# Kernel optimization log

Measured on AMD Instinct MI355X. Metric: run time of the kernel, lower is better.

The kernel has to match this reference:

```python
import jax, jax.numpy as jnp
import numpy as np

N = 50000      # nodes of type 'conn'
E = 250000     # edges per edge type
NT = 3         # number of edge types
H = 3          # num_heads for hidden layers
D1, D2, DO = 64, 64, 32
IN0 = 34       # 8 + 3 + 6 + 17


def setup_inputs() -> dict:
    key = jax.random.key(0)
    ks = jax.random.split(key, 40)
    it = iter(range(40))

    def nrm(shape, scale=0.1):
        return jax.random.normal(ks[next(it)], shape, dtype=jnp.float32) * scale

    inp = {}
    inp["cat_inputs"] = jax.random.randint(ks[next(it)], (N, 3), 0, 5, dtype=jnp.int32)
    inp["cont_inputs"] = jax.random.normal(ks[next(it)], (N, 17), dtype=jnp.float32)
    inp["src"] = jax.random.randint(ks[next(it)], (NT, E), 0, N)
    inp["dst"] = jax.random.randint(ks[next(it)], (NT, E), 0, N)
    # embedding tables
    inp["emb0"] = nrm((14, 8))
    inp["emb1"] = nrm((5, 3))
    inp["emb2"] = nrm((10, 6))
    # layer 1: GATConv(34 -> 64, heads=3) per etype
    inp["W1"] = nrm((NT, IN0, H * D1))
    inp["al1"] = nrm((NT, H, D1))
    inp["ar1"] = nrm((NT, H, D1))
    inp["b1"] = nrm((NT, H * D1))
    # layer 2: GATConv(192 -> 64, heads=3) per etype
    inp["W2"] = nrm((NT, H * D1, H * D2))
    inp["al2"] = nrm((NT, H, D2))
    inp["ar2"] = nrm((NT, H, D2))
    inp["b2"] = nrm((NT, H * D2))
    # output layer: GATConv(192 -> 32, heads=1) per etype
    inp["W3"] = nrm((NT, H * D2, DO))
    inp["al3"] = nrm((NT, 1, DO))
    inp["ar3"] = nrm((NT, 1, DO))
    inp["b3"] = nrm((NT, DO))
    return inp


def _gat(x, W, al, ar, b, src_t, dst_t, heads, out):
    """DGL GATConv: linear -> per-edge LeakyReLU(0.2) attention -> edge softmax
    over incoming edges -> weighted scatter-sum -> +bias -> leaky_relu(0.01)."""
    n = x.shape[0]
    feat = (x @ W).reshape(n, heads, out)          # (N,H,D)
    el = jnp.sum(feat * al, axis=-1)               # (N,H)
    er = jnp.sum(feat * ar, axis=-1)               # (N,H)
    e = jax.nn.leaky_relu(el[src_t] + er[dst_t], 0.2)  # (E,H)
    emax = jax.ops.segment_max(e, dst_t, num_segments=n)   # (N,H), -inf for empty ok
    ee = jnp.exp(e - emax[dst_t])
    den = jax.ops.segment_sum(ee, dst_t, num_segments=n)
    alpha = ee / den[dst_t]                        # (E,H)
    msg = feat[src_t] * alpha[:, :, None]          # (E,H,D)
    rst = jax.ops.segment_sum(msg, dst_t, num_segments=n) + b.reshape(1, heads, out)
    return jax.nn.leaky_relu(rst, 0.01)            # GATConv activation=F.leaky_relu


def reference(cont_inputs, emb0, emb1, emb2,
              W1, al1, ar1, b1, W2, al2, ar2, b2, W3, al3, ar3, b3,
              cat_inputs, src, dst):
    x = jnp.concatenate([emb0[cat_inputs[:, 0]],
                         emb1[cat_inputs[:, 1]],
                         emb2[cat_inputs[:, 2]],
                         cont_inputs], axis=1)     # (N,34)

    def hetero(h, W, al, ar, b, heads, out):
        # HeteroGraphConv(aggregate='mean') over NT edge types, then flatten(1)
        outs = [_gat(h, W[t], al[t], ar[t], b[t], src[t], dst[t], heads, out)
                for t in range(NT)]
        agg = jnp.mean(jnp.stack(outs, 0), axis=0)  # (N,heads,out)
        return agg.reshape(h.shape[0], heads * out)

    h = hetero(x, W1, al1, ar1, b1, H, D1)
    h = hetero(h, W2, al2, ar2, b2, H, D2)
    h = hetero(h, W3, al3, ar3, b3, 1, DO)
    return h
```

## Files before the change

### kernel.cpp

```cpp
#include <hip/hip_runtime.h>

#define NNODES 50000
#define NEDGES 250000
#define NTYPES 3
#define SCAN_B ((NNODES + 255) / 256)

typedef __attribute__((ext_vector_type(8))) short bf16x8;
typedef __attribute__((ext_vector_type(4))) float f32x4;

__device__ __forceinline__ float lrelu(float x, float s) { return x >= 0.f ? x : s * x; }

__device__ __forceinline__ unsigned short bf16_rne(float f) {
    unsigned u = __float_as_uint(f);
    unsigned r = (u + 0x7fffu + ((u >> 16) & 1u)) >> 16;
    return (unsigned short)r;
}
__device__ __forceinline__ float bf16_to_f(unsigned short h) {
    return __uint_as_float((unsigned)h << 16);
}

__global__ void build_x_kernel(const int* __restrict__ cat, const float* __restrict__ cont,
                               const float* __restrict__ e0, const float* __restrict__ e1,
                               const float* __restrict__ e2, short* __restrict__ Ahi,
                               short* __restrict__ Alo) {
    int n = blockIdx.x * 4 + (threadIdx.x >> 6);
    int k = threadIdx.x & 63;
    if (n >= NNODES) return;
    float v = 0.f;
    if (k < 8) v = e0[cat[n * 3 + 0] * 8 + k];
    else if (k < 11) v = e1[cat[n * 3 + 1] * 3 + (k - 8)];
    else if (k < 17) v = e2[cat[n * 3 + 2] * 6 + (k - 11)];
    else if (k < 34) v = cont[n * 17 + (k - 17)];
    unsigned short h = bf16_rne(v);
    float fh = bf16_to_f(h);
    unsigned short l = bf16_rne(v - fh);
    Ahi[(size_t)n * 64 + k] = (short)h;
    Alo[(size_t)n * 64 + k] = (short)l;
}

__global__ void hist_kernel(const int* __restrict__ dst, int* __restrict__ deg) {
    int idx = blockIdx.x * blockDim.x + threadIdx.x;
    if (idx >= NTYPES * NEDGES) return;
    int t = idx / NEDGES;
    atomicAdd(&deg[t * NNODES + dst[idx]], 1);
}

__global__ void scan1_kernel(const int* __restrict__ deg, int* __restrict__ rowptr,
                             int* __restrict__ bsum) {
    __shared__ int sd[256];
    int t = blockIdx.y, b = blockIdx.x, tid = threadIdx.x;
    int n = b * 256 + tid;
    int v = (n < NNODES) ? deg[t * NNODES + n] : 0;
    sd[tid] = v;
    __syncthreads();
    for (int off = 1; off < 256; off <<= 1) {
        int x = 0;
        if (tid >= off) x = sd[tid - off];
        __syncthreads();
        if (tid >= off) sd[tid] += x;
        __syncthreads();
    }
    int incl = sd[tid];
    if (n < NNODES) rowptr[(size_t)t * (NNODES + 1) + n] = incl - v;
    if (tid == 255) bsum[t * SCAN_B + b] = incl;
}

__global__ void scan2_kernel(int* __restrict__ bsum, int* __restrict__ rowptr) {
    int t = threadIdx.x;
    if (t >= NTYPES) return;
    int run = 0;
    for (int i = 0; i < SCAN_B; i++) {
        int v = bsum[t * SCAN_B + i];
        bsum[t * SCAN_B + i] = run;
        run += v;
    }
    rowptr[(size_t)t * (NNODES + 1) + NNODES] = run;
}

__global__ void scan3_kernel(const int* __restrict__ bsum, int* __restrict__ rowptr) {
    int t = blockIdx.y, b = blockIdx.x;
    int n = b * 256 + threadIdx.x;
    if (n < NNODES) rowptr[(size_t)t * (NNODES + 1) + n] += bsum[t * SCAN_B + b];
}

__global__ void scatter_kernel(const int* __restrict__ src, const int* __restrict__ dst,
                               const int* __restrict__ rowptr, int* __restrict__ cursor,
                               int* __restrict__ csrc) {
    int idx = blockIdx.x * blockDim.x + threadIdx.x;
    if (idx >= NTYPES * NEDGES) return;
    int t = idx / NEDGES;
    int s = src[idx], d = dst[idx];
    int pos = rowptr[(size_t)t * (NNODES + 1) + d] + atomicAdd(&cursor[t * NNODES + d], 1);
    csrc[(size_t)t * NEDGES + pos] = s;
}

__global__ void convert_B_kernel(const float* __restrict__ W, short* __restrict__ Bhi,
                                 short* __restrict__ Blo, int Kin, int Kout, int HD, int Mfeat) {
    int idx = blockIdx.x * blockDim.x + threadIdx.x;
    if (idx >= Mfeat * Kout) return;
    int m = idx / Kout, k = idx % Kout;
    int t = m / HD, j = m % HD;
    float a = (k < Kin) ? W[((size_t)t * Kin + k) * HD + j] : 0.f;
    unsigned short h = bf16_rne(a);
    float fh = bf16_to_f(h);
    unsigned short l = bf16_rne(a - fh);
    Bhi[(size_t)m * Kout + k] = (short)h;
    Blo[(size_t)m * Kout + k] = (short)l;
}

__global__ void convert_Bel_kernel(const float* __restrict__ W, const float* __restrict__ alw,
                                   const float* __restrict__ arw, short* __restrict__ Bhi,
                                   short* __restrict__ Blo, int Kin, int Kout, int H, int D,
                                   int Mfeat) {
    int idx = blockIdx.x * blockDim.x + threadIdx.x;
    if (idx >= 24 * Kout) return;
    int m = idx / Kout, k = idx % Kout;
    int t = m >> 3, r = m & 7;
    int h = r & 3;
    float v = 0.f;
    if (h < H && k < Kin) {
        const float* a = ((r >= 4) ? arw : alw) + ((size_t)t * H + h) * D;
        const float* w = W + ((size_t)t * Kin + k) * (H * D) + h * D;
        for (int j = 0; j < D; j++) v += w[j] * a[j];
    }
    unsigned short hh = bf16_rne(v);
    float fh = bf16_to_f(hh);
    unsigned short ll = bf16_rne(v - fh);
    size_t o = (size_t)(Mfeat + m) * Kout + k;
    Bhi[o] = (short)hh;
    Blo[o] = (short)ll;
}

__global__ __launch_bounds__(256) void gemm_mfma_kernel(
    const short* __restrict__ AhiG, const short* __restrict__ AloG,
    const short* __restrict__ BhiG, const short* __restrict__ BloG,
    unsigned short* __restrict__ feat, float* __restrict__ elr, int N, int K, int M, int Mfeat,
    int HD, size_t tstride) {
    __shared__ short smem[4 * 128 * 40];
    short* AsH = smem;
    short* AsL = smem + 128 * 40;
    short* BsH = smem + 2 * 128 * 40;
    short* BsL = smem + 3 * 128 * 40;
    int tid = threadIdx.x;
    int m0 = blockIdx.x * 128, n0 = blockIdx.y * 128;
    int wid = tid >> 6, lane = tid & 63;
    int wm = (wid >> 1) * 64, wn = (wid & 1) * 64;
    int lrow = lane & 15, kq = (lane >> 4) * 8;
    f32x4 acc[4][4] = {};

    for (int k0 = 0; k0 < K; k0 += 32) {
        __syncthreads();
#pragma unroll
        for (int p = 0; p < 2; p++) {
            int r = (tid >> 2) + p * 64;
            int kq2 = (tid & 3) * 8;
            bf16x8 z = {};
            bf16x8 vh = z, vl = z;
            int gr = n0 + r;
            if (gr < N) {
                size_t o = (size_t)gr * K + k0 + kq2;
                vh = *(const bf16x8*)(AhiG + o);
                vl = *(const bf16x8*)(AloG + o);
            }
            *(bf16x8*)&AsH[r * 40 + kq2] = vh;
            *(bf16x8*)&AsL[r * 40 + kq2] = vl;
            vh = z;
            vl = z;
            int gc = m0 + r;
            if (gc < M) {
                size_t o = (size_t)gc * K + k0 + kq2;
                vh = *(const bf16x8*)(BhiG + o);
                vl = *(const bf16x8*)(BloG + o);
            }
            *(bf16x8*)&BsH[r * 40 + kq2] = vh;
            *(bf16x8*)&BsL[r * 40 + kq2] = vl;
        }
        __syncthreads();
        bf16x8 ah[4], al[4], bh[4], bl[4];
#pragma unroll
        for (int f = 0; f < 4; f++) {
            int ra = (wm + f * 16 + lrow) * 40 + kq;
            ah[f] = *(const bf16x8*)&AsH[ra];
            al[f] = *(const bf16x8*)&AsL[ra];
            int rb = (wn + f * 16 + lrow) * 40 + kq;
            bh[f] = *(const bf16x8*)&BsH[rb];
            bl[f] = *(const bf16x8*)&BsL[rb];
        }
#pragma unroll
        for (int fa = 0; fa < 4; fa++)
#pragma unroll
            for (int fb = 0; fb < 4; fb++) {
                acc[fa][fb] =
                    __builtin_amdgcn_mfma_f32_16x16x32_bf16(al[fa], bh[fb], acc[fa][fb], 0, 0, 0);
                acc[fa][fb] =
                    __builtin_amdgcn_mfma_f32_16x16x32_bf16(ah[fa], bl[fb], acc[fa][fb], 0, 0, 0);
                acc[fa][fb] =
                    __builtin_amdgcn_mfma_f32_16x16x32_bf16(ah[fa], bh[fb], acc[fa][fb], 0, 0, 0);
            }
    }

    __syncthreads();
    short* Ct = smem;
#pragma unroll
    for (int fb = 0; fb < 4; fb++) {
        int col = wn + fb * 16 + lrow;
        int gc = m0 + col;
#pragma unroll
        for (int fa = 0; fa < 4; fa++) {
            int rbase = wm + fa * 16 + (lane >> 4) * 4;
#pragma unroll
            for (int e = 0; e < 4; e++) {
                Ct[(rbase + e) * 136 + col] = (short)bf16_rne(acc[fa][fb][e]);
                if (gc >= Mfeat && gc < M) {
                    int gr = n0 + rbase + e;
                    if (gr < N) {
                        int m = gc - Mfeat;
                        int t = m >> 3, r = m & 7;
                        elr[((size_t)t * N + gr) * 8 + r] = acc[fa][fb][e];
                    }
                }
            }
        }
    }
    __syncthreads();
    int row = tid >> 1, half = tid & 1;
    int gr = n0 + row;
    if (gr < N) {
#pragma unroll
        for (int p = 0; p < 4; p++) {
            int col0 = half * 64 + p * 16;
            int gc0 = m0 + col0;
            if (gc0 < Mfeat) {
                int t = gc0 / HD, j = gc0 - t * HD;
                bf16x8 v0 = *(const bf16x8*)&Ct[row * 136 + col0];
                bf16x8 v1 = *(const bf16x8*)&Ct[row * 136 + col0 + 8];
                unsigned short* dp = feat + (size_t)t * tstride + (size_t)gr * HD + j;
                *(bf16x8*)dp = v0;
                *(bf16x8*)(dp + 8) = v1;
            }
        }
    }
}

template <int H>
__global__ void alpha_kernel(const int* __restrict__ rowptr_all, const int* __restrict__ csrc_all,
                             const float* __restrict__ elr, float* __restrict__ alpha_all) {
    int idx = blockIdx.x * blockDim.x + threadIdx.x;
    if (idx >= NTYPES * NNODES) return;
    int t = idx / NNODES, node = idx - t * NNODES;
    const int* rowptr = rowptr_all + t * (NNODES + 1);
    const int* csrc = csrc_all + (size_t)t * NEDGES;
    const float* elr_t = elr + (size_t)t * NNODES * 8;
    float4* alpha4 = (float4*)(alpha_all + (size_t)t * NEDGES * 4);
    float4 er4 = *(const float4*)(elr_t + (size_t)node * 8 + 4);
    float erd[3] = {er4.x, er4.y, er4.z};
    int rs = rowptr[node], re = rowptr[node + 1];
    float den[H];
#pragma unroll
    for (int h = 0; h < H; h++) den[h] = 0.f;
    for (int k = rs; k < re; k++) {
        int s = csrc[k];
        float4 e4 = *(const float4*)(elr_t + (size_t)s * 8);
        float ev[3] = {e4.x, e4.y, e4.z};
        float w[4] = {0.f, 0.f, 0.f, 0.f};
#pragma unroll
        for (int h = 0; h < H; h++) {
            w[h] = __expf(lrelu(ev[h] + erd[h], 0.2f));
            den[h] += w[h];
        }
        alpha4[k] = (float4){w[0], w[1], w[2], w[3]};
    }
    float inv[H];
#pragma unroll
    for (int h = 0; h < H; h++) inv[h] = __frcp_rn(den[h]);
    for (int k = rs; k < re; k++) {
        float4 w = alpha4[k];
        w.x *= inv[0];
        if (H > 1) {
            w.y *= inv[1];
            w.z *= inv[2];
        }
        alpha4[k] = w;
    }
}

template <int H, int D, int BF16OUT>
__global__ __launch_bounds__(256) void gat_agg_kernel(
    const int* __restrict__ rowptr_all, const int* __restrict__ csrc_all,
    const float* __restrict__ alpha_all, const unsigned short* __restrict__ feat_all,
    const float* __restrict__ b_all, float* __restrict__ fout, short* __restrict__ Ahi,
    short* __restrict__ Alo) {
    constexpr int HD = H * D;
    constexpr int EL = (HD + 63) / 64;
    int lane = threadIdx.x & 63;
    int node = blockIdx.x * 4 + (threadIdx.x >> 6);
    if (node >= NNODES) return;
    float out[EL] = {};
#pragma unroll 1
    for (int t = 0; t < NTYPES; t++) {
        const int* rowptr = rowptr_all + t * (NNODES + 1);
        const int* csrc = csrc_all + (size_t)t * NEDGES;
        const float4* alpha4 = (const float4*)(alpha_all + (size_t)t * NEDGES * 4);
        const unsigned short* feat = feat_all + (size_t)t * NNODES * HD;
        int rs = rowptr[node], re = rowptr[node + 1];
        float acc[EL] = {};
        for (int k = rs; k < re; k += 4) {
            int cnt = re - k;
            int s[4];
            float4 w4[4];
#pragma unroll
            for (int c = 0; c < 4; c++) {
                s[c] = csrc[k + (c < cnt ? c : 0)];
                w4[c] = (c < cnt) ? alpha4[k + c] : (float4){0.f, 0.f, 0.f, 0.f};
            }
#pragma unroll
            for (int c = 0; c < 4; c++) {
                float wv[3] = {w4[c].x, w4[c].y, w4[c].z};
#pragma unroll
                for (int q = 0; q < EL; q++) {
                    int j = lane + q * 64;
                    constexpr bool full = (HD % 64 == 0);
                    float fv = 0.f;
                    if (full || lane < (HD % 64) || q < EL - 1)
                        fv = bf16_to_f(feat[(size_t)s[c] * HD + j]);
                    int hh = (D == 64) ? q : 0;
                    acc[q] = fmaf(wv[hh], fv, acc[q]);
                }
            }
        }
#pragma unroll
        for (int q = 0; q < EL; q++) {
            int j = lane + q * 64;
            if (HD % 64 == 0 || j < HD) {
                float v = lrelu(acc[q] + b_all[t * HD + j], 0.01f);
                out[q] += v * (1.f / 3.f);
            }
        }
    }
#pragma unroll
    for (int q = 0; q < EL; q++) {
        int j = lane + q * 64;
        if (HD % 64 == 0 || j < HD) {
            if (BF16OUT) {
                unsigned short h = bf16_rne(out[q]);
                float fh = bf16_to_f(h);
                unsigned short l = bf16_rne(out[q] - fh);
                Ahi[(size_t)node * HD + j] = (short)h;
                Alo[(size_t)node * HD + j] = (short)l;
            } else {
                fout[(size_t)node * HD + j] = out[q];
            }
        }
    }
}

extern "C" void kernel_launch(void* const* d_in, const int* in_sizes, int n_in, void* d_out,
                              int out_size, void* d_ws, size_t ws_size, hipStream_t stream) {
    const int* cat = (const int*)d_in[0];
    const float* cont = (const float*)d_in[1];
    const int* src = (const int*)d_in[2];
    const int* dst = (const int*)d_in[3];
    const float* emb0 = (const float*)d_in[4];
    const float* emb1 = (const float*)d_in[5];
    const float* emb2 = (const float*)d_in[6];
    const float* W1 = (const float*)d_in[7];
    const float* al1 = (const float*)d_in[8];
    const float* ar1 = (const float*)d_in[9];
    const float* b1 = (const float*)d_in[10];
    const float* W2 = (const float*)d_in[11];
    const float* al2 = (const float*)d_in[12];
    const float* ar2 = (const float*)d_in[13];
    const float* b2 = (const float*)d_in[14];
    const float* W3 = (const float*)d_in[15];
    const float* al3 = (const float*)d_in[16];
    const float* ar3 = (const float*)d_in[17];
    const float* b3 = (const float*)d_in[18];

    unsigned short* feat_all = (unsigned short*)d_ws;
    short* Ahi = (short*)(feat_all + (size_t)3 * NNODES * 192);
    short* Alo = Ahi + (size_t)NNODES * 192;
    short* Bhi = Alo + (size_t)NNODES * 192;
    short* Blo = Bhi + 600 * 192;
    float* elr = (float*)(Blo + 600 * 192);
    float* alpha_all = elr + (size_t)3 * NNODES * 8;
    int* rowptr = (int*)(alpha_all + (size_t)3 * NEDGES * 4);
    int* csrc = rowptr + NTYPES * (NNODES + 1);
    int* deg = csrc + NTYPES * NEDGES;
    int* cursor = deg + NTYPES * NNODES;
    int* bsum = cursor + NTYPES * NNODES;

    hipMemsetAsync(deg, 0, (size_t)NTYPES * NNODES * 4, stream);
    hipMemsetAsync(cursor, 0, (size_t)NTYPES * NNODES * 4, stream);
    hist_kernel<<<(NTYPES * NEDGES + 255) / 256, 256, 0, stream>>>(dst, deg);
    scan1_kernel<<<dim3(SCAN_B, NTYPES), 256, 0, stream>>>(deg, rowptr, bsum);
    scan2_kernel<<<1, 64, 0, stream>>>(bsum, rowptr);
    scan3_kernel<<<dim3(SCAN_B, NTYPES), 256, 0, stream>>>(bsum, rowptr);
    scatter_kernel<<<(NTYPES * NEDGES + 255) / 256, 256, 0, stream>>>(src, dst, rowptr, cursor,
                                                                      csrc);

    build_x_kernel<<<(NNODES + 3) / 4, 256, 0, stream>>>(cat, cont, emb0, emb1, emb2, Ahi, Alo);

    const int gy = (NNODES + 127) / 128;
    const int aggb = (NNODES + 3) / 4;
    const int nb = (NTYPES * NNODES + 255) / 256;

    convert_B_kernel<<<(576 * 64 + 255) / 256, 256, 0, stream>>>(W1, Bhi, Blo, 34, 64, 192, 576);
    convert_Bel_kernel<<<(24 * 64 + 255) / 256, 256, 0, stream>>>(W1, al1, ar1, Bhi, Blo, 34, 64, 3,
                                                                  64, 576);
    gemm_mfma_kernel<<<dim3(5, gy), 256, 0, stream>>>(Ahi, Alo, Bhi, Blo, feat_all, elr, NNODES, 64,
                                                      600, 576, 192, (size_t)NNODES * 192);
    alpha_kernel<3><<<nb, 256, 0, stream>>>(rowptr, csrc, elr, alpha_all);
    gat_agg_kernel<3, 64, 1><<<aggb, 256, 0, stream>>>(rowptr, csrc, alpha_all, feat_all, b1,
                                                       nullptr, Ahi, Alo);

    convert_B_kernel<<<(576 * 192 + 255) / 256, 256, 0, stream>>>(W2, Bhi, Blo, 192, 192, 192, 576);
    convert_Bel_kernel<<<(24 * 192 + 255) / 256, 256, 0, stream>>>(W2, al2, ar2, Bhi, Blo, 192, 192,
                                                                   3, 64, 576);
    gemm_mfma_kernel<<<dim3(5, gy), 256, 0, stream>>>(Ahi, Alo, Bhi, Blo, feat_all, elr, NNODES,
                                                      192, 600, 576, 192, (size_t)NNODES * 192);
    alpha_kernel<3><<<nb, 256, 0, stream>>>(rowptr, csrc, elr, alpha_all);
    gat_agg_kernel<3, 64, 1><<<aggb, 256, 0, stream>>>(rowptr, csrc, alpha_all, feat_all, b2,
                                                       nullptr, Ahi, Alo);

    convert_B_kernel<<<(96 * 192 + 255) / 256, 256, 0, stream>>>(W3, Bhi, Blo, 192, 192, 32, 96);
    convert_Bel_kernel<<<(24 * 192 + 255) / 256, 256, 0, stream>>>(W3, al3, ar3, Bhi, Blo, 192, 192,
                                                                   1, 32, 96);
    gemm_mfma_kernel<<<dim3(1, gy), 256, 0, stream>>>(Ahi, Alo, Bhi, Blo, feat_all, elr, NNODES,
                                                      192, 120, 96, 32, (size_t)NNODES * 32);
    alpha_kernel<1><<<nb, 256, 0, stream>>>(rowptr, csrc, elr, alpha_all);
    gat_agg_kernel<1, 32, 0><<<aggb, 256, 0, stream>>>(rowptr, csrc, alpha_all, feat_all, b3,
                                                       (float*)d_out, nullptr, nullptr);
}
```

Before: 553.9 us.

## Prefetch next GEMM K-tile into registers and remap workgroups across XCDs

The MFMA GEMM now loads the next K-slice of A and B into registers while computing on the current LDS tile, then stores it after a barrier. This overlaps global loads with MFMA work. The launch becomes a 1D grid with a swizzle that gives each of the 8 XCDs a contiguous range of tiles, so neighbouring tiles share L2. The LDS row stride drops from 40 to 36 shorts. This adds register pressure, and the new stride may change bank-conflict behaviour.

```diff
diff --git a/kernel.cpp b/kernel.cpp
--- a/kernel.cpp
+++ b/kernel.cpp
@@ -4,6 +4,7 @@
 #define NEDGES 250000
 #define NTYPES 3
 #define SCAN_B ((NNODES + 255) / 256)
+#define LSTR 36
 
 typedef __attribute__((ext_vector_type(8))) short bf16x8;
 typedef __attribute__((ext_vector_type(4))) float f32x4;
@@ -135,54 +136,67 @@
     const short* __restrict__ AhiG, const short* __restrict__ AloG,
     const short* __restrict__ BhiG, const short* __restrict__ BloG,
     unsigned short* __restrict__ feat, float* __restrict__ elr, int N, int K, int M, int Mfeat,
-    int HD, size_t tstride) {
-    __shared__ short smem[4 * 128 * 40];
+    int HD, size_t tstride, int MT) {
+    __shared__ short smem[4 * 128 * LSTR];
     short* AsH = smem;
-    short* AsL = smem + 128 * 40;
-    short* BsH = smem + 2 * 128 * 40;
-    short* BsL = smem + 3 * 128 * 40;
+    short* AsL = smem + 128 * LSTR;
+    short* BsH = smem + 2 * 128 * LSTR;
+    short* BsL = smem + 3 * 128 * LSTR;
     int tid = threadIdx.x;
-    int m0 = blockIdx.x * 128, n0 = blockIdx.y * 128;
+
+    int nwg = gridDim.x;
+    int q = nwg >> 3, rr = nwg & 7;
+    int x = blockIdx.x & 7, i = blockIdx.x >> 3;
+    int wg = (x < rr ? x * (q + 1) : rr * (q + 1) + (x - rr) * q) + i;
+    int m0 = (wg % MT) * 128, n0 = (wg / MT) * 128;
+
     int wid = tid >> 6, lane = tid & 63;
     int wm = (wid >> 1) * 64, wn = (wid & 1) * 64;
     int lrow = lane & 15, kq = (lane >> 4) * 8;
+    int sr = tid >> 2;
+    int skq = (tid & 3) * 8;
     f32x4 acc[4][4] = {};
+    bf16x8 rg[8];
+
+    auto load_tile = [&](int k0) {
+        const bf16x8 z = {};
+#pragma unroll
+        for (int p = 0; p < 2; p++) {
+            int gr = n0 + sr + p * 64;
+            int gc = m0 + sr + p * 64;
+            size_t oa = (size_t)gr * K + k0 + skq;
+            size_t ob = (size_t)gc * K + k0 + skq;
+            rg[p * 4 + 0] = (gr < N) ? *(const bf16x8*)(AhiG + oa) : z;
+            rg[p * 4 + 1] = (gr < N) ? *(const bf16x8*)(AloG + oa) : z;
+            rg[p * 4 + 2] = (gc < M) ? *(const bf16x8*)(BhiG + ob) : z;
+            rg[p * 4 + 3] = (gc < M) ? *(const bf16x8*)(BloG + ob) : z;
+        }
+    };
+    auto store_tile = [&]() {
+#pragma unroll
+        for (int p = 0; p < 2; p++) {
+            int r = sr + p * 64;
+            *(bf16x8*)&AsH[r * LSTR + skq] = rg[p * 4 + 0];
+            *(bf16x8*)&AsL[r * LSTR + skq] = rg[p * 4 + 1];
+            *(bf16x8*)&BsH[r * LSTR + skq] = rg[p * 4 + 2];
+            *(bf16x8*)&BsL[r * LSTR + skq] = rg[p * 4 + 3];
+        }
+    };
+
+    load_tile(0);
+    store_tile();
+    __syncthreads();
 
     for (int k0 = 0; k0 < K; k0 += 32) {
-        __syncthreads();
-#pragma unroll
-        for (int p = 0; p < 2; p++) {
-            int r = (tid >> 2) + p * 64;
-            int kq2 = (tid & 3) * 8;
-            bf16x8 z = {};
-            bf16x8 vh = z, vl = z;
-            int gr = n0 + r;
-            if (gr < N) {
-                size_t o = (size_t)gr * K + k0 + kq2;
-                vh = *(const bf16x8*)(AhiG + o);
-                vl = *(const bf16x8*)(AloG + o);
-            }
-            *(bf16x8*)&AsH[r * 40 + kq2] = vh;
-            *(bf16x8*)&AsL[r * 40 + kq2] = vl;
-            vh = z;
-            vl = z;
-            int gc = m0 + r;
-            if (gc < M) {
-                size_t o = (size_t)gc * K + k0 + kq2;
-                vh = *(const bf16x8*)(BhiG + o);
-                vl = *(const bf16x8*)(BloG + o);
-            }
-            *(bf16x8*)&BsH[r * 40 + kq2] = vh;
-            *(bf16x8*)&BsL[r * 40 + kq2] = vl;
-        }
-        __syncthreads();
+        bool has_next = (k0 + 32 < K);
+        if (has_next) load_tile(k0 + 32);
         bf16x8 ah[4], al[4], bh[4], bl[4];
 #pragma unroll
         for (int f = 0; f < 4; f++) {
-            int ra = (wm + f * 16 + lrow) * 40 + kq;
+            int ra = (wm + f * 16 + lrow) * LSTR + kq;
             ah[f] = *(const bf16x8*)&AsH[ra];
             al[f] = *(const bf16x8*)&AsL[ra];
-            int rb = (wn + f * 16 + lrow) * 40 + kq;
+            int rb = (wn + f * 16 + lrow) * LSTR + kq;
             bh[f] = *(const bf16x8*)&BsH[rb];
             bl[f] = *(const bf16x8*)&BsL[rb];
         }
@@ -197,9 +211,13 @@
                 acc[fa][fb] =
                     __builtin_amdgcn_mfma_f32_16x16x32_bf16(ah[fa], bh[fb], acc[fa][fb], 0, 0, 0);
             }
-    }
-
-    __syncthreads();
+        __syncthreads();
+        if (has_next) {
+            store_tile();
+            __syncthreads();
+        }
+    }
+
     short* Ct = smem;
 #pragma unroll
     for (int fb = 0; fb < 4; fb++) {
@@ -407,8 +425,8 @@
     convert_B_kernel<<<(576 * 64 + 255) / 256, 256, 0, stream>>>(W1, Bhi, Blo, 34, 64, 192, 576);
     convert_Bel_kernel<<<(24 * 64 + 255) / 256, 256, 0, stream>>>(W1, al1, ar1, Bhi, Blo, 34, 64, 3,
                                                                   64, 576);
-    gemm_mfma_kernel<<<dim3(5, gy), 256, 0, stream>>>(Ahi, Alo, Bhi, Blo, feat_all, elr, NNODES, 64,
-                                                      600, 576, 192, (size_t)NNODES * 192);
+    gemm_mfma_kernel<<<5 * gy, 256, 0, stream>>>(Ahi, Alo, Bhi, Blo, feat_all, elr, NNODES, 64, 600,
+                                                 576, 192, (size_t)NNODES * 192, 5);
     alpha_kernel<3><<<nb, 256, 0, stream>>>(rowptr, csrc, elr, alpha_all);
     gat_agg_kernel<3, 64, 1><<<aggb, 256, 0, stream>>>(rowptr, csrc, alpha_all, feat_all, b1,
                                                        nullptr, Ahi, Alo);
@@ -416,8 +434,8 @@
     convert_B_kernel<<<(576 * 192 + 255) / 256, 256, 0, stream>>>(W2, Bhi, Blo, 192, 192, 192, 576);
     convert_Bel_kernel<<<(24 * 192 + 255) / 256, 256, 0, stream>>>(W2, al2, ar2, Bhi, Blo, 192, 192,
                                                                    3, 64, 576);
-    gemm_mfma_kernel<<<dim3(5, gy), 256, 0, stream>>>(Ahi, Alo, Bhi, Blo, feat_all, elr, NNODES,
-                                                      192, 600, 576, 192, (size_t)NNODES * 192);
+    gemm_mfma_kernel<<<5 * gy, 256, 0, stream>>>(Ahi, Alo, Bhi, Blo, feat_all, elr, NNODES, 192,
+                                                 600, 576, 192, (size_t)NNODES * 192, 5);
     alpha_kernel<3><<<nb, 256, 0, stream>>>(rowptr, csrc, elr, alpha_all);
     gat_agg_kernel<3, 64, 1><<<aggb, 256, 0, stream>>>(rowptr, csrc, alpha_all, feat_all, b2,
                                                        nullptr, Ahi, Alo);
@@ -425,8 +443,8 @@
     convert_B_kernel<<<(96 * 192 + 255) / 256, 256, 0, stream>>>(W3, Bhi, Blo, 192, 192, 32, 96);
     convert_Bel_kernel<<<(24 * 192 + 255) / 256, 256, 0, stream>>>(W3, al3, ar3, Bhi, Blo, 192, 192,
                                                                    1, 32, 96);
-    gemm_mfma_kernel<<<dim3(1, gy), 256, 0, stream>>>(Ahi, Alo, Bhi, Blo, feat_all, elr, NNODES,
-                                                      192, 120, 96, 32, (size_t)NNODES * 32);
+    gemm_mfma_kernel<<<1 * gy, 256, 0, stream>>>(Ahi, Alo, Bhi, Blo, feat_all, elr, NNODES, 192,
+                                                 120, 96, 32, (size_t)NNODES * 32, 1);
     alpha_kernel<1><<<nb, 256, 0, stream>>>(rowptr, csrc, elr, alpha_all);
     gat_agg_kernel<1, 32, 0><<<aggb, 256, 0, stream>>>(rowptr, csrc, alpha_all, feat_all, b3,
                                                        (float*)d_out, nullptr, nullptr);
```

Result: slower. 687.5 us (+24.1%).
